# Kernel optimization log

Measured on AMD Instinct MI355X. Metric: run time of the kernel, lower is better.

## Reference

```python
import jax, jax.numpy as jnp
from jax import lax
import numpy as np

# HH / synapse constants (CFG in original repo; standard values matching the rate eqns)
GNA, GK, GL = 40.0, 35.0, 0.3
ENA, EK, EL = 55.0, -77.0, -65.0
GS, VS = 1.0, 0.0
IAPP = 1.0
VT, KP = -20.0, 3.0
A_D, A_R = 1.0, 0.1
DT = 0.02

B, N, L = 16, 2000, 1024


def setup_inputs() -> dict:
    key = jax.random.key(0)
    z = jax.random.uniform(key, (B, N, L), dtype=jnp.float32)
    return {"z": z}


def _rates(V):
    # Singularity-safe rate constants (the torch code patches V==25 / V==-35 exactly).
    at25 = V == 25.0
    atm35 = V == -35.0
    dN = jnp.where(at25, 1.0, 1.0 - jnp.exp((-V + 25.0) / 9.0))
    dM = jnp.where(atm35, 1.0, 1.0 - jnp.exp((-V - 35.0) / 9.0))
    dNb = jnp.where(at25, 1.0, 1.0 - jnp.exp((V - 25.0) / 9.0))
    dMb = jnp.where(atm35, 1.0, 1.0 - jnp.exp((V + 35.0) / 9.0))
    aN = jnp.where(at25, 0.18, 0.02 * (V - 25.0) / dN)
    bN = jnp.where(at25, 0.08, -0.002 * (V - 25.0) / dNb)
    aM = jnp.where(atm35, 1.638, 0.182 * (V + 35.0) / dM)
    bM = jnp.where(atm35, 1.16, -0.124 * (V + 35.0) / dMb)
    aH = 0.25 * jnp.exp((-V - 90.0) / 12.0)
    bH = 0.25 * jnp.exp((V + 34.0) / 12.0)
    return aN, bN, aM, bM, aH, bH


def _step(carry, z_prev):
    V, m, n, h, y = carry
    pow1 = GNA * m ** 3 * h
    pow2 = GK * n ** 4
    G = DT / 2 * (pow1 + pow2 + GL + GS * y)
    E = pow1 * ENA + pow2 * EK + GL * EL + GS * VS * y
    Vn = (V * (1.0 - G) + DT * (E + IAPP)) / (1.0 + G)
    aN, bN, aM, bM, aH, bH = _rates(Vn)
    mn = (aM * DT + (1.0 - DT / 2 * (aM + bM)) * m) / (DT / 2 * (aM + bM) + 1.0)
    nn = (aN * DT + (1.0 - DT / 2 * (aN + bN)) * n) / (DT / 2 * (aN + bN) + 1.0)
    hn = (aH * DT + (1.0 - DT / 2 * (aH + bH)) * h) / (DT / 2 * (aH + bH) + 1.0)
    ady = A_D * z_prev
    yn = (ady * DT + (1.0 - DT / 2 * (ady + A_R)) * y) / (DT / 2 * (ady + A_R) + 1.0)
    return (Vn, mn, nn, hn, yn), Vn


def _hh(z):
    b, n_t, l = z.shape
    zt = jnp.moveaxis(z, 1, 0)  # (N, B, L); step k uses z[k-1]
    V0 = jnp.full((b, l), -70.0, dtype=z.dtype)
    zeros = jnp.zeros((b, l), dtype=z.dtype)
    ones = jnp.ones((b, l), dtype=z.dtype)
    carry0 = (V0, zeros, zeros, ones, zeros)
    _, Vseq = lax.scan(_step, carry0, zt[:-1])  # (N-1, B, L)
    Vall = jnp.concatenate([V0[None], Vseq], axis=0)  # (N, B, L)
    V = jnp.moveaxis(Vall, 0, 1)  # (B, N, L)
    return jax.nn.sigmoid((V - VT) / KP)


def reference(z):
    return _hh(z)
```

## Files before the change

kernel.cpp:

```cpp
#include <hip/hip_runtime.h>

#define N_ 2000
#define L_ 1024

__device__ __forceinline__ float rcpf(float d) { return __builtin_amdgcn_rcpf(d); }
__device__ __forceinline__ float ex2(float x)  { return __builtin_amdgcn_exp2f(x); }

#define STEP1(K, RS)                                                          \
  {                                                                           \
    const int kk = (K);                                                       \
    float zc = zb[RS];                                                        \
    int kpre = kk + 7;                                                        \
    int kc = kpre < 1998 ? kpre : 1998;                                       \
    zb[RS] = z[base + kc * L_];                                               \
                                                       \
    float mh   = m * h;                                                       \
    float m2   = m * m;                                                       \
    float valm = m2 * mh;                                          \
    float n2   = n * n;                                                       \
    float valn = n2 * n2;                                          \
    float gy   = __fmaf_rn(y, 0.01f, 0.003f);                                 \
    float G    = __fmaf_rn(valm, 0.4f, __fmaf_rn(valn, 0.35f, gy));           \
    float E    = __fmaf_rn(valm, 2200.0f, __fmaf_rn(valn, -2695.0f, -19.5f)); \
    float rV   = rcpf(1.0f + G);                                              \
    float tVD  = __fmaf_rn(E, 0.02f, __fmaf_rn(2.0f, V, 0.02f));              \
    float Vn   = __fmaf_rn(tVD, rV, -V);          \
                                      \
    float eRm  = ex2(__fmaf_rn(Vn, K9, 35.0f * K9));       \
    float eRn  = eRm * CN;                                 \
    float dm   = eRm - 1.0f;                                                  \
    float dn   = eRn - 1.0f;                                                  \
    bool patm  = (Vn == -35.0f);                                              \
    bool patn  = (Vn == 25.0f);                                               \
    float dmS  = patm ? 1.0f : dm;        \
    float dnS  = patn ? 1.0f : dn;        \
    float rp   = rcpf(dmS * dnS);                                             \
    float rrm  = rp * dnS;                                                    \
    float rrn  = rp * dmS;                                                    \
    float um   = Vn + 35.0f;                                                  \
    float un   = Vn - 25.0f;                                                  \
    float urm  = um * rrm;                                                    \
    float urn  = un * rrn;                                                    \
    float sm   = urm * __fmaf_rn(0.00182f, eRm, 0.00124f);                    \
    float sn   = urn * __fmaf_rn(0.0002f,  eRn, 0.00002f);                    \
    float aM   = 0.182f * (urm * eRm);                                        \
    float aN   = 0.02f  * (urn * eRn);                                        \
    sm = patm ? 0.02798f : sm;  aM = patm ? 1.638f : aM;                      \
    sn = patn ? 0.0026f  : sn;  aN = patn ? 0.18f  : aN;                      \
                                      \
    float aH   = 0.25f * ex2(__fmaf_rn(Vn, -K12, -90.0f * K12));              \
    float bH   = 0.25f * ex2(__fmaf_rn(Vn,  K12,  34.0f * K12));              \
    float sh   = __fmaf_rn(aH, 0.01f, 0.01f * bH);                            \
    float sy   = __fmaf_rn(zc, 0.01f, 0.001f);                                \
    float qm = 1.0f + sm, qn = 1.0f + sn, qh = 1.0f + sh, qy = 1.0f + sy;     \
    float numm = __fmaf_rn(aM, 0.02f, __fmaf_rn(-sm, m, m));                  \
    float numn = __fmaf_rn(aN, 0.02f, __fmaf_rn(-sn, n, n));                  \
    float numh = __fmaf_rn(aH, 0.02f, __fmaf_rn(-sh, h, h));                  \
    float numy = __fmaf_rn(zc, 0.02f, __fmaf_rn(-sy, y, y));                  \
       \
    float e2 = eRm * eRm;                                                     \
    float ts = (e2 * eRm) * 0.006737946999085467f;                            \
    float uS = 1.0f + ts;                                                     \
                                  \
    float t1 = qm * qn;                                                       \
    float t2 = qh * qy;                                                       \
    float t12 = t1 * t2;                                                      \
    float rall = rcpf(t12 * uS);                                              \
    float rq  = rall * uS;                                     \
    float rs  = rall * t12;                                    \
    float rmn = rq * t2;                                       \
    float rhy = rq * t1;                                       \
    m = numm * (rmn * qn);                                                    \
    n = numn * (rmn * qm);                                                    \
    h = numh * (rhy * qy);                                                    \
    y = numy * (rhy * qh);                                                    \
    V = Vn;                                                                   \
    float sg = ts * rs;                                                       \
    out[base + kk * L_] = sg;                                                 \
  }

__global__ __launch_bounds__(64) void hh_kernel(const float* __restrict__ z,
                                                float* __restrict__ out) {
    const int t   = blockIdx.x * 64 + threadIdx.x;
    const int b   = t >> 10;
    const int l   = t & 1023;
    const int base = b * (N_ * L_) + l;

    const float K9  = 0.16029944898766259f;
    const float K12 = 0.12022458674074695f;
    const float CN  = 0.0012726338013398079f;

    float V = -70.0f;
    float m = 0.0f, n = 0.0f, h = 1.0f, y = 0.0f;

    float zb[8];
#pragma unroll
    for (int i = 0; i < 8; ++i) zb[i] = z[base + i * L_];

    out[base] = 5.777750e-8f;

    int k = 1;
    for (int g = 0; g < 249; ++g) {
#pragma unroll
        for (int j = 0; j < 8; ++j) {
            STEP1(k + j, j)
        }
        k += 8;
    }
#pragma unroll
    for (int j = 0; j < 7; ++j) {
        STEP1(k + j, j)
    }
}

extern "C" void kernel_launch(void* const* d_in, const int* in_sizes, int n_in,
                              void* d_out, int out_size, void* d_ws, size_t ws_size,
                              hipStream_t stream) {
    const float* z = (const float*)d_in[0];
    float* out = (float*)d_out;
    hh_kernel<<<256, 64, 0, stream>>>(z, out);
}
```

Measured before the change: 495.4 us.

## Replace batched reciprocals with independent rcps and fold rate constants into exponents

Reworks the per-step HH update so each gate denominator gets its own reciprocal instead of a single shared reciprocal with a multiply tree. Constants such as 0.25 and 0.01 are folded into the exp2 offsets so the h-gate terms need fewer multiplies. The prefetch clamp is removed from the main loop by peeling the last groups, and the batch row offset is made wave-uniform via readfirstlane so addressing can use scalar registers. This trades more rcp instructions (transcendental throughput) for a shorter dependency chain and fewer VALU ops on the serial critical path.

```diff
diff --git a/kernel.cpp b/kernel.cpp
--- a/kernel.cpp
+++ b/kernel.cpp
@@ -6,110 +6,110 @@
 __device__ __forceinline__ float rcpf(float d) { return __builtin_amdgcn_rcpf(d); }
 __device__ __forceinline__ float ex2(float x)  { return __builtin_amdgcn_exp2f(x); }
 
-#define STEP1(K, RS)                                                          \
+#define STEP1(K, RS, PRE)                                                     \
   {                                                                           \
     const int kk = (K);                                                       \
     float zc = zb[RS];                                                        \
-    int kpre = kk + 7;                                                        \
-    int kc = kpre < 1998 ? kpre : 1998;                                       \
-    zb[RS] = z[base + kc * L_];                                               \
-                                                       \
+    if ((PRE) == 0) {                                                         \
+      zb[RS] = (zrow + (kk + 7) * L_)[lu];                                    \
+    } else if ((PRE) == 1) {                                                  \
+      int kc = kk + 7; kc = kc < 1998 ? kc : 1998;                            \
+      zb[RS] = (zrow + kc * L_)[lu];                                          \
+    }                                                                         \
+                                                            \
     float mh   = m * h;                                                       \
     float m2   = m * m;                                                       \
     float valm = m2 * mh;                                          \
     float n2   = n * n;                                                       \
-    float valn = n2 * n2;                                          \
+    float valn = n2 * n2;                                           \
     float gy   = __fmaf_rn(y, 0.01f, 0.003f);                                 \
     float G    = __fmaf_rn(valm, 0.4f, __fmaf_rn(valn, 0.35f, gy));           \
     float E    = __fmaf_rn(valm, 2200.0f, __fmaf_rn(valn, -2695.0f, -19.5f)); \
     float rV   = rcpf(1.0f + G);                                              \
     float tVD  = __fmaf_rn(E, 0.02f, __fmaf_rn(2.0f, V, 0.02f));              \
-    float Vn   = __fmaf_rn(tVD, rV, -V);          \
-                                      \
+    float Vn   = __fmaf_rn(tVD, rV, -V);         \
+               \
     float eRm  = ex2(__fmaf_rn(Vn, K9, 35.0f * K9));       \
-    float eRn  = eRm * CN;                                 \
     float dm   = eRm - 1.0f;                                                  \
-    float dn   = eRn - 1.0f;                                                  \
-    bool patm  = (Vn == -35.0f);                                              \
-    bool patn  = (Vn == 25.0f);                                               \
-    float dmS  = patm ? 1.0f : dm;        \
-    float dnS  = patn ? 1.0f : dn;        \
-    float rp   = rcpf(dmS * dnS);                                             \
-    float rrm  = rp * dnS;                                                    \
-    float rrn  = rp * dmS;                                                    \
+    float dn   = __fmaf_rn(CN, eRm, -1.0f);                      \
     float um   = Vn + 35.0f;                                                  \
     float un   = Vn - 25.0f;                                                  \
+    float rrm  = rcpf(dm);                                                    \
+    float rrn  = rcpf(dn);                                                    \
     float urm  = um * rrm;                                                    \
     float urn  = un * rrn;                                                    \
     float sm   = urm * __fmaf_rn(0.00182f, eRm, 0.00124f);                    \
-    float sn   = urn * __fmaf_rn(0.0002f,  eRn, 0.00002f);                    \
-    float aM   = 0.182f * (urm * eRm);                                        \
-    float aN   = 0.02f  * (urn * eRn);                                        \
-    sm = patm ? 0.02798f : sm;  aM = patm ? 1.638f : aM;                      \
-    sn = patn ? 0.0026f  : sn;  aN = patn ? 0.18f  : aN;                      \
-                                      \
-    float aH   = 0.25f * ex2(__fmaf_rn(Vn, -K12, -90.0f * K12));              \
-    float bH   = 0.25f * ex2(__fmaf_rn(Vn,  K12,  34.0f * K12));              \
-    float sh   = __fmaf_rn(aH, 0.01f, 0.01f * bH);                            \
+    float sn   = urn * __fmaf_rn(KXN, eRm, 0.00002f);                         \
+    float tm   = urm * eRm;                                                   \
+    float tn   = urn * eRm;                                                   \
+    bool patm  = (Vn == -35.0f);                                              \
+    bool patn  = (Vn == 25.0f);                                               \
+    sm = patm ? 0.02798f : sm;   tm = patm ? 9.0f   : tm;                     \
+    sn = patn ? 0.0026f  : sn;   tn = patn ? TNPAT  : tn;                     \
+                                   \
+    float A    = ex2(__fmaf_rn(Vn, -K12, CAH));                               \
+    float Bv   = ex2(__fmaf_rn(Vn,  K12, CBH));                               \
+    float sh   = A + Bv;                                                      \
     float sy   = __fmaf_rn(zc, 0.01f, 0.001f);                                \
-    float qm = 1.0f + sm, qn = 1.0f + sn, qh = 1.0f + sh, qy = 1.0f + sy;     \
-    float numm = __fmaf_rn(aM, 0.02f, __fmaf_rn(-sm, m, m));                  \
-    float numn = __fmaf_rn(aN, 0.02f, __fmaf_rn(-sn, n, n));                  \
-    float numh = __fmaf_rn(aH, 0.02f, __fmaf_rn(-sh, h, h));                  \
-    float numy = __fmaf_rn(zc, 0.02f, __fmaf_rn(-sy, y, y));                  \
-       \
+                                          \
+    float numm = __fmaf_rn(tm, 0.00364f, __fmaf_rn(-sm, m, m));               \
+    float numn = __fmaf_rn(tn, KAN,      __fmaf_rn(-sn, n, n));               \
+    float numh = __fmaf_rn(A,  2.0f,     __fmaf_rn(-sh, h, h));               \
+    float numy = __fmaf_rn(zc, 0.02f,    __fmaf_rn(-sy, y, y));               \
+    m = numm * rcpf(1.0f + sm);                                               \
+    n = numn * rcpf(1.0f + sn);                                               \
+    h = numh * rcpf(1.0f + sh);                                               \
+    y = numy * rcpf(1.0f + sy);                                               \
+    V = Vn;                                                                   \
+                                     \
     float e2 = eRm * eRm;                                                     \
     float ts = (e2 * eRm) * 0.006737946999085467f;                            \
-    float uS = 1.0f + ts;                                                     \
-                                  \
-    float t1 = qm * qn;                                                       \
-    float t2 = qh * qy;                                                       \
-    float t12 = t1 * t2;                                                      \
-    float rall = rcpf(t12 * uS);                                              \
-    float rq  = rall * uS;                                     \
-    float rs  = rall * t12;                                    \
-    float rmn = rq * t2;                                       \
-    float rhy = rq * t1;                                       \
-    m = numm * (rmn * qn);                                                    \
-    n = numn * (rmn * qm);                                                    \
-    h = numh * (rhy * qy);                                                    \
-    y = numy * (rhy * qh);                                                    \
-    V = Vn;                                                                   \
-    float sg = ts * rs;                                                       \
-    out[base + kk * L_] = sg;                                                 \
+    float sg = ts * rcpf(1.0f + ts);                                          \
+    (orow + kk * L_)[lu] = sg;                                                \
   }
 
 __global__ __launch_bounds__(64) void hh_kernel(const float* __restrict__ z,
                                                 float* __restrict__ out) {
-    const int t   = blockIdx.x * 64 + threadIdx.x;
-    const int b   = t >> 10;
-    const int l   = t & 1023;
-    const int base = b * (N_ * L_) + l;
+    const int t  = blockIdx.x * 64 + threadIdx.x;
+    const int bu = __builtin_amdgcn_readfirstlane(t >> 10);
+    const int lu = t & 1023;
+
+    const float* zrow = z   + (size_t)bu * (N_ * L_);
+    float*       orow = out + (size_t)bu * (N_ * L_);
 
     const float K9  = 0.16029944898766259f;
     const float K12 = 0.12022458674074695f;
     const float CN  = 0.0012726338013398079f;
+    const float KXN = 2.5452676026796158e-7f;
+    const float KAN = 5.0905352053592316e-7f;
+    const float TNPAT = 7071.948f;
+    const float CAH = -19.46406899644195f;
+    const float CBH = -4.556220240589328f;
 
     float V = -70.0f;
     float m = 0.0f, n = 0.0f, h = 1.0f, y = 0.0f;
 
     float zb[8];
 #pragma unroll
-    for (int i = 0; i < 8; ++i) zb[i] = z[base + i * L_];
+    for (int i = 0; i < 8; ++i) zb[i] = (zrow + i * L_)[lu];
 
-    out[base] = 5.777750e-8f;
+    orow[lu] = 5.777750e-8f;
 
     int k = 1;
-    for (int g = 0; g < 249; ++g) {
+    for (int g = 0; g < 248; ++g) {
 #pragma unroll
         for (int j = 0; j < 8; ++j) {
-            STEP1(k + j, j)
+            STEP1(k + j, j, 0)
         }
         k += 8;
     }
 #pragma unroll
+    for (int j = 0; j < 8; ++j) {
+        STEP1(1985 + j, j, 1)
+    }
+#pragma unroll
     for (int j = 0; j < 7; ++j) {
-        STEP1(k + j, j)
+        STEP1(1993 + j, j, 2)
     }
 }
 
```

Measured after the change: 478.5 us (median of 2 runs). 3.4% less time.
